# Optimization experiments

Hardware: AMD Instinct MI355X
Metric: run time of the kernel (lower is better)

Reference implementation:

```python
import jax, jax.numpy as jnp
import numpy as np

VOCAB, EMBED, HIDDEN = 32000, 256, 64
B, T = 4096, 64


def setup_inputs() -> dict:
    key = jax.random.key(0)
    ks = jax.random.split(key, 6)
    s = 1.0 / float(np.sqrt(HIDDEN))  # PyTorch LSTM init scale
    x = jax.random.randint(ks[0], (B, T), 0, VOCAB)
    embed_table = jax.random.normal(ks[1], (VOCAB, EMBED), jnp.float32)
    W_ih = jax.random.uniform(ks[2], (4 * HIDDEN, EMBED), jnp.float32, -s, s)
    W_hh = jax.random.uniform(ks[3], (4 * HIDDEN, HIDDEN), jnp.float32, -s, s)
    b_ih = jax.random.uniform(ks[4], (4 * HIDDEN,), jnp.float32, -s, s)
    b_hh = jax.random.uniform(ks[5], (4 * HIDDEN,), jnp.float32, -s, s)
    return {"x": x, "embed_table": embed_table, "W_ih": W_ih, "W_hh": W_hh, "b_ih": b_ih, "b_hh": b_hh}


def reference(x, embed_table, W_ih, W_hh, b_ih, b_hh):
    # Embedding lookup: [B,T,E]
    emb = embed_table[x]
    # Precompute input projection for all timesteps (PyTorch gate order i,f,g,o)
    xg = jnp.einsum('bte,ge->btg', emb, W_ih) + (b_ih + b_hh)  # [B,T,4H]
    xg = jnp.swapaxes(xg, 0, 1)  # [T,B,4H]
    h0 = jnp.zeros((x.shape[0], HIDDEN), xg.dtype)
    c0 = jnp.zeros((x.shape[0], HIDDEN), xg.dtype)

    def step(carry, xt):
        h, c = carry
        g = xt + h @ W_hh.T  # [B,4H]
        i, f, gg, o = jnp.split(g, 4, axis=-1)
        c = jax.nn.sigmoid(f) * c + jax.nn.sigmoid(i) * jnp.tanh(gg)
        h = jax.nn.sigmoid(o) * jnp.tanh(c)
        return (h, c), None

    (h, _), _ = jax.lax.scan(step, (h0, c0), xg)
    return h  # [B, HIDDEN] == hidden.squeeze(0)
```

## Files before the change

### kernel.cpp

```cpp
#include <hip/hip_runtime.h>
#include <math.h>

#define B_ 4096
#define T_ 64
#define E_ 256
#define H_ 64
#define V_ 32000
#define THREADS 1024

typedef __attribute__((ext_vector_type(8))) short bf16x8;
typedef __attribute__((ext_vector_type(4))) float f32x4;
typedef __attribute__((ext_vector_type(4))) unsigned int u32x4;

__device__ __forceinline__ short f2bf(float x) {
    unsigned u = __float_as_uint(x);
    return (short)((u + 0x7FFFu + ((u >> 16) & 1u)) >> 16);
}
__device__ __forceinline__ unsigned cvt_pk_bf16(float lo, float hi) {
    unsigned r;
    asm("v_cvt_pk_bf16_f32 %0, %1, %2" : "=v"(r) : "v"(lo), "v"(hi));
    return r;
}
__device__ __forceinline__ float exp2_raw(float x) {
    float r; asm("v_exp_f32 %0, %1" : "=v"(r) : "v"(x)); return r;
}
__device__ __forceinline__ float rcp_raw(float x) {
    float r; asm("v_rcp_f32 %0, %1" : "=v"(r) : "v"(x)); return r;
}
#define LOG2E 1.442695041f

__device__ __forceinline__ void gld16(const void* g, void* l) {
    __builtin_amdgcn_global_load_lds(
        (const __attribute__((address_space(1))) void*)g,
        (__attribute__((address_space(3))) void*)l, 16, 0, 0);
}

__global__ void prep_kernel(const float* __restrict__ W_ih,
                            const float* __restrict__ W_hh,
                            const float* __restrict__ b_ih,
                            const float* __restrict__ b_hh,
                            const float* __restrict__ emb_table,
                            short* __restrict__ wih_frag,
                            short* __restrict__ whh_g,
                            float* __restrict__ bias_f,
                            short* __restrict__ emb_bf,
                            int tabN) {
    int tid = blockIdx.x * blockDim.x + threadIdx.x;
    int stride = gridDim.x * blockDim.x;
    for (int i = tid; i < 65536; i += stride) {
        int jj = i & 7;
        int l  = (i >> 3) & 63;
        int kc = (i >> 9) & 7;
        int tl = (i >> 12) & 1;
        int vv = i >> 13;
        int uu = (l & 15) >> 1, pp = l & 1;
        int g = tl * 128 + pp * 64 + vv * 8 + uu;
        int k = kc * 32 + (l >> 4) * 8 + jj;
        wih_frag[i] = f2bf(W_ih[g * E_ + k]);
    }
    for (int i = tid; i < 256 * 64; i += stride) whh_g[i] = f2bf(W_hh[i]);
    for (int i = tid; i < 256; i += stride) bias_f[i] = b_ih[i] + b_hh[i];
    for (int i = tid; i < (tabN >> 2); i += stride) {
        float4 v = ((const float4*)emb_table)[i];
        uint2 w;
        w.x = cvt_pk_bf16(v.x, v.y);
        w.y = cvt_pk_bf16(v.z, v.w);
        ((uint2*)emb_bf)[i] = w;
    }
}

template <int TAB>
__global__ __attribute__((amdgpu_flat_work_group_size(THREADS, THREADS),
                          amdgpu_waves_per_eu(4, 4)))
void lstm_f(const int* __restrict__ x,
            const float* __restrict__ embf,
            const short* __restrict__ embb,
            const short* __restrict__ wih_frag,
            const short* __restrict__ whh_g,
            const float* __restrict__ bias_f,
            float* __restrict__ out) {
    __shared__ __align__(16) short s_ef[4][4096];
    __shared__ __align__(16) short s_hf[2][1024];
    __shared__ int s_idx[1024];

    const int tid  = threadIdx.x;
    const int lane = tid & 63;
    const int wave = tid >> 6;
    const int r0   = blockIdx.x * 16;

    s_idx[(tid & 63) * 16 + (tid >> 6)] = x[(r0 + (tid >> 6)) * T_ + (tid & 63)];
    ((int*)s_hf)[tid] = 0;

    const int p  = lane & 1;
    const int c4 = lane >> 4;
    const int u  = (lane & 15) >> 1;
    const float scl2 = p ? 1.0f : 2.0f;
    const float offB = p ? 0.0f : -1.0f;
    const float enB  = -LOG2E * scl2;
    const int m0 = c4 * 4 + p * 2;

    bf16x8 wA[8], wB[8], qA0, qA1, qB0, qB1;
    float bA = 0.f, bB = 0.f;
    int hw_s = 0;
    if (wave < 8) {
        const short* wp = wih_frag + wave * 8192 + lane * 8;
        #pragma unroll
        for (int kc = 0; kc < 8; ++kc) {
            wA[kc] = *(const bf16x8*)(wp + kc * 512);
            wB[kc] = *(const bf16x8*)(wp + 4096 + kc * 512);
        }
        const int gA = p * 64 + wave * 8 + u;
        const short* qp = whh_g + gA * 64 + c4 * 8;
        qA0 = *(const bf16x8*)(qp);
        qA1 = *(const bf16x8*)(qp + 32);
        qB0 = *(const bf16x8*)(qp + 8192);
        qB1 = *(const bf16x8*)(qp + 8192 + 32);
        bA = bias_f[gA];
        bB = bias_f[gA + 128];
        hw_s = (wave >> 2) * 512 + (wave & 3) * 128
             + ((u & 1) ? (m0 + 1) * 8 + (u - 1) : m0 * 8 + u);
    }

    const int m16   = lane & 15;
    const int sbase = (wave - 8) * 512 + lane * 8;
    const int skoff = (wave - 8) * 32 + (lane >> 4) * 8;

    __syncthreads();

    if (wave >= 8) {
        #pragma unroll
        for (int tt = 0; tt < 2; ++tt) {
            int tok = s_idx[tt * 16 + m16];
            if (TAB) {
                gld16(embb + (size_t)tok * E_ + skoff,
                      &s_ef[tt][(wave - 8) * 512]);
            } else {
                const float* pr = embf + (size_t)tok * E_ + skoff;
                float4 f0 = *(const float4*)pr;
                float4 f1 = *(const float4*)(pr + 4);
                u32x4 w;
                w[0] = cvt_pk_bf16(f0.x, f0.y);
                w[1] = cvt_pk_bf16(f0.z, f0.w);
                w[2] = cvt_pk_bf16(f1.x, f1.y);
                w[3] = cvt_pk_bf16(f1.z, f1.w);
                *(u32x4*)(&s_ef[tt][0] + sbase) = w;
            }
        }
    }
    __syncthreads();

    f32x4 pA, pB;
    if (wave < 8) {
        pA = (f32x4){bA, bA, bA, bA};
        pB = (f32x4){bB, bB, bB, bB};
        const short* eb = &s_ef[0][0] + lane * 8;
        #pragma unroll
        for (int kc = 0; kc < 8; ++kc) {
            bf16x8 av = *(const bf16x8*)(eb + kc * 512);
            pA = __builtin_amdgcn_mfma_f32_16x16x32_bf16(av, wA[kc], pA, 0, 0, 0);
            pB = __builtin_amdgcn_mfma_f32_16x16x32_bf16(av, wB[kc], pB, 0, 0, 0);
        }
    }

    float c0 = 0.f, c1 = 0.f, h0v = 0.f, h1v = 0.f;

    #pragma unroll 4
    for (int t = 0; t < T_; ++t) {
        if (wave < 8) {
            const short* hb = &s_hf[t & 1][0] + lane * 8;
            bf16x8 hv0 = *(const bf16x8*)(hb);
            bf16x8 hv1 = *(const bf16x8*)(hb + 512);
            pA = __builtin_amdgcn_mfma_f32_16x16x32_bf16(hv0, qA0, pA, 0, 0, 0);
            pA = __builtin_amdgcn_mfma_f32_16x16x32_bf16(hv1, qA1, pA, 0, 0, 0);
            pB = __builtin_amdgcn_mfma_f32_16x16x32_bf16(hv0, qB0, pB, 0, 0, 0);
            pB = __builtin_amdgcn_mfma_f32_16x16x32_bf16(hv1, qB1, pB, 0, 0, 0);

            float sA[4], Bv[4];
            #pragma unroll
            for (int q = 0; q < 4; ++q) {
                sA[q] = rcp_raw(1.0f + exp2_raw(-LOG2E * pA[q]));
                Bv[q] = rcp_raw(1.0f + exp2_raw(enB * pB[q])) * scl2 + offB;
            }
            float s1 = p ? sA[0] : sA[2] * Bv[2];
            float r1 = __shfl_xor(s1, 1);
            float s2 = p ? sA[1] : sA[3] * Bv[3];
            float r2 = __shfl_xor(s2, 1);
            float r3 = __shfl_xor(Bv[0], 1);
            float r4 = __shfl_xor(Bv[1], 1);
            float fc0 = p ? sA[2] : r1;
            float ic0 = p ? r1 : sA[0] * Bv[0];
            float oc0 = p ? Bv[2] : r3;
            float fc1 = p ? sA[3] : r2;
            float ic1 = p ? r2 : sA[1] * Bv[1];
            float oc1 = p ? Bv[3] : r4;
            c0 = fc0 * c0 + ic0;
            c1 = fc1 * c1 + ic1;
            h0v = oc0 * (1.0f - 2.0f * rcp_raw(1.0f + exp2_raw(2.0f * LOG2E * c0)));
            h1v = oc1 * (1.0f - 2.0f * rcp_raw(1.0f + exp2_raw(2.0f * LOG2E * c1)));

            float snd = (u & 1) ? h0v : h1v;
            float rcv = __shfl_xor(snd, 2);
            unsigned hw = (u & 1) ? cvt_pk_bf16(rcv, h1v) : cvt_pk_bf16(h0v, rcv);
            *(unsigned*)(&s_hf[(t + 1) & 1][0] + hw_s) = hw;

            if (t < T_ - 1) {
                pA = (f32x4){bA, bA, bA, bA};
                pB = (f32x4){bB, bB, bB, bB};
                const short* eb = &s_ef[(t + 1) & 3][0] + lane * 8;
                #pragma unroll
                for (int kc = 0; kc < 8; ++kc) {
                    bf16x8 av = *(const bf16x8*)(eb + kc * 512);
                    pA = __builtin_amdgcn_mfma_f32_16x16x32_bf16(av, wA[kc], pA, 0, 0, 0);
                    pB = __builtin_amdgcn_mfma_f32_16x16x32_bf16(av, wB[kc], pB, 0, 0, 0);
                }
            }
        } else {
            if (t + 2 < T_) {
                int tok = s_idx[(t + 2) * 16 + m16];
                if (TAB) {
                    gld16(embb + (size_t)tok * E_ + skoff,
                          &s_ef[(t + 2) & 3][(wave - 8) * 512]);
                } else {
                    const float* pr = embf + (size_t)tok * E_ + skoff;
                    float4 f0 = *(const float4*)pr;
                    float4 f1 = *(const float4*)(pr + 4);
                    u32x4 w;
                    w[0] = cvt_pk_bf16(f0.x, f0.y);
                    w[1] = cvt_pk_bf16(f0.z, f0.w);
                    w[2] = cvt_pk_bf16(f1.x, f1.y);
                    w[3] = cvt_pk_bf16(f1.z, f1.w);
                    *(u32x4*)(&s_ef[(t + 2) & 3][0] + sbase) = w;
                }
            }
        }
        __syncthreads();
    }

    if (wave < 8) {
        const int j = wave * 8 + u;
        out[(r0 + m0) * H_ + j]     = h0v;
        out[(r0 + m0 + 1) * H_ + j] = h1v;
    }
}

extern "C" void kernel_launch(void* const* d_in, const int* in_sizes, int n_in,
                              void* d_out, int out_size, void* d_ws, size_t ws_size,
                              hipStream_t stream) {
    const int*   x         = (const int*)d_in[0];
    const float* emb_table = (const float*)d_in[1];
    const float* W_ih      = (const float*)d_in[2];
    const float* W_hh      = (const float*)d_in[3];
    const float* b_ih      = (const float*)d_in[4];
    const float* b_hh      = (const float*)d_in[5];
    float*       out       = (float*)d_out;

    short* wih_frag = (short*)d_ws;
    short* whh_g    = wih_frag + 65536;
    float* bias_f   = (float*)(whh_g + 16384);
    short* emb_bf   = (short*)(bias_f + 256);

    const size_t need = (size_t)(65536 + 16384) * 2 + 256 * 4
                      + (size_t)V_ * E_ * 2;
    const int tab = (ws_size >= need) ? 1 : 0;

    prep_kernel<<<tab ? 1024 : 64, 256, 0, stream>>>(
        W_ih, W_hh, b_ih, b_hh, emb_table,
        wih_frag, whh_g, bias_f,
        tab ? emb_bf : wih_frag, tab ? V_ * E_ : 0);

    if (tab) {
        lstm_f<1><<<B_ / 16, THREADS, 0, stream>>>(
            x, emb_table, emb_bf, wih_frag, whh_g, bias_f, out);
    } else {
        lstm_f<0><<<B_ / 16, THREADS, 0, stream>>>(
            x, emb_table, wih_frag, wih_frag, whh_g, bias_f, out);
    }
}
```

Baseline: 75.05 us.

## Deepen embedding prefetch to three steps and split MFMA accumulators into two chains

The loader waves now prefetch embedding rows three timesteps ahead instead of two. On the async-load path, the full syncthreads is replaced by a partial vmcnt(1) wait plus a raw barrier, so one global load can stay in flight across the barrier. Each gate accumulator is split into two independent MFMA chains that are summed before the activations, which shortens the dependent MFMA chain on the recurrent critical path. This adds some VALU adds and registers, and it depends on the relaxed wait count being correct for the four-slot ring buffer.

```diff
diff --git a/kernel.cpp b/kernel.cpp
--- a/kernel.cpp
+++ b/kernel.cpp
@@ -129,7 +129,7 @@
 
     if (wave >= 8) {
         #pragma unroll
-        for (int tt = 0; tt < 2; ++tt) {
+        for (int tt = 0; tt < 3; ++tt) {
             int tok = s_idx[tt * 16 + m16];
             if (TAB) {
                 gld16(embb + (size_t)tok * E_ + skoff,
@@ -147,18 +147,29 @@
             }
         }
     }
-    __syncthreads();
-
-    f32x4 pA, pB;
+    if (TAB) {
+        asm volatile("s_waitcnt vmcnt(1) lgkmcnt(0)" ::: "memory");
+        __builtin_amdgcn_s_barrier();
+        __builtin_amdgcn_sched_barrier(0);
+    } else {
+        __syncthreads();
+    }
+
+    f32x4 a0, a1, b0, b1;
     if (wave < 8) {
-        pA = (f32x4){bA, bA, bA, bA};
-        pB = (f32x4){bB, bB, bB, bB};
+        a0 = (f32x4){bA, bA, bA, bA};
+        b0 = (f32x4){bB, bB, bB, bB};
+        a1 = (f32x4){0.f, 0.f, 0.f, 0.f};
+        b1 = (f32x4){0.f, 0.f, 0.f, 0.f};
         const short* eb = &s_ef[0][0] + lane * 8;
         #pragma unroll
-        for (int kc = 0; kc < 8; ++kc) {
+        for (int kc = 0; kc < 4; ++kc) {
             bf16x8 av = *(const bf16x8*)(eb + kc * 512);
-            pA = __builtin_amdgcn_mfma_f32_16x16x32_bf16(av, wA[kc], pA, 0, 0, 0);
-            pB = __builtin_amdgcn_mfma_f32_16x16x32_bf16(av, wB[kc], pB, 0, 0, 0);
+            bf16x8 aw = *(const bf16x8*)(eb + (kc + 4) * 512);
+            a0 = __builtin_amdgcn_mfma_f32_16x16x32_bf16(av, wA[kc], a0, 0, 0, 0);
+            b0 = __builtin_amdgcn_mfma_f32_16x16x32_bf16(av, wB[kc], b0, 0, 0, 0);
+            a1 = __builtin_amdgcn_mfma_f32_16x16x32_bf16(aw, wA[kc + 4], a1, 0, 0, 0);
+            b1 = __builtin_amdgcn_mfma_f32_16x16x32_bf16(aw, wB[kc + 4], b1, 0, 0, 0);
         }
     }
 
@@ -170,16 +181,18 @@
             const short* hb = &s_hf[t & 1][0] + lane * 8;
             bf16x8 hv0 = *(const bf16x8*)(hb);
             bf16x8 hv1 = *(const bf16x8*)(hb + 512);
-            pA = __builtin_amdgcn_mfma_f32_16x16x32_bf16(hv0, qA0, pA, 0, 0, 0);
-            pA = __builtin_amdgcn_mfma_f32_16x16x32_bf16(hv1, qA1, pA, 0, 0, 0);
-            pB = __builtin_amdgcn_mfma_f32_16x16x32_bf16(hv0, qB0, pB, 0, 0, 0);
-            pB = __builtin_amdgcn_mfma_f32_16x16x32_bf16(hv1, qB1, pB, 0, 0, 0);
+            a0 = __builtin_amdgcn_mfma_f32_16x16x32_bf16(hv0, qA0, a0, 0, 0, 0);
+            a1 = __builtin_amdgcn_mfma_f32_16x16x32_bf16(hv1, qA1, a1, 0, 0, 0);
+            b0 = __builtin_amdgcn_mfma_f32_16x16x32_bf16(hv0, qB0, b0, 0, 0, 0);
+            b1 = __builtin_amdgcn_mfma_f32_16x16x32_bf16(hv1, qB1, b1, 0, 0, 0);
 
             float sA[4], Bv[4];
             #pragma unroll
             for (int q = 0; q < 4; ++q) {
-                sA[q] = rcp_raw(1.0f + exp2_raw(-LOG2E * pA[q]));
-                Bv[q] = rcp_raw(1.0f + exp2_raw(enB * pB[q])) * scl2 + offB;
+                float gaq = a0[q] + a1[q];
+                float gbq = b0[q] + b1[q];
+                sA[q] = rcp_raw(1.0f + exp2_raw(-LOG2E * gaq));
+                Bv[q] = rcp_raw(1.0f + exp2_raw(enB * gbq)) * scl2 + offB;
             }
             float s1 = p ? sA[0] : sA[2] * Bv[2];
             float r1 = __shfl_xor(s1, 1);
@@ -204,22 +217,27 @@
             *(unsigned*)(&s_hf[(t + 1) & 1][0] + hw_s) = hw;
 
             if (t < T_ - 1) {
-                pA = (f32x4){bA, bA, bA, bA};
-                pB = (f32x4){bB, bB, bB, bB};
+                a0 = (f32x4){bA, bA, bA, bA};
+                b0 = (f32x4){bB, bB, bB, bB};
+                a1 = (f32x4){0.f, 0.f, 0.f, 0.f};
+                b1 = (f32x4){0.f, 0.f, 0.f, 0.f};
                 const short* eb = &s_ef[(t + 1) & 3][0] + lane * 8;
                 #pragma unroll
-                for (int kc = 0; kc < 8; ++kc) {
+                for (int kc = 0; kc < 4; ++kc) {
                     bf16x8 av = *(const bf16x8*)(eb + kc * 512);
-                    pA = __builtin_amdgcn_mfma_f32_16x16x32_bf16(av, wA[kc], pA, 0, 0, 0);
-                    pB = __builtin_amdgcn_mfma_f32_16x16x32_bf16(av, wB[kc], pB, 0, 0, 0);
+                    bf16x8 aw = *(const bf16x8*)(eb + (kc + 4) * 512);
+                    a0 = __builtin_amdgcn_mfma_f32_16x16x32_bf16(av, wA[kc], a0, 0, 0, 0);
+                    b0 = __builtin_amdgcn_mfma_f32_16x16x32_bf16(av, wB[kc], b0, 0, 0, 0);
+                    a1 = __builtin_amdgcn_mfma_f32_16x16x32_bf16(aw, wA[kc + 4], a1, 0, 0, 0);
+                    b1 = __builtin_amdgcn_mfma_f32_16x16x32_bf16(aw, wB[kc + 4], b1, 0, 0, 0);
                 }
             }
         } else {
-            if (t + 2 < T_) {
-                int tok = s_idx[(t + 2) * 16 + m16];
+            if (t + 3 < T_) {
+                int tok = s_idx[(t + 3) * 16 + m16];
                 if (TAB) {
                     gld16(embb + (size_t)tok * E_ + skoff,
-                          &s_ef[(t + 2) & 3][(wave - 8) * 512]);
+                          &s_ef[(t + 3) & 3][(wave - 8) * 512]);
                 } else {
                     const float* pr = embf + (size_t)tok * E_ + skoff;
                     float4 f0 = *(const float4*)pr;
@@ -229,11 +247,17 @@
                     w[1] = cvt_pk_bf16(f0.z, f0.w);
                     w[2] = cvt_pk_bf16(f1.x, f1.y);
                     w[3] = cvt_pk_bf16(f1.z, f1.w);
-                    *(u32x4*)(&s_ef[(t + 2) & 3][0] + sbase) = w;
+                    *(u32x4*)(&s_ef[(t + 3) & 3][0] + sbase) = w;
                 }
             }
         }
-        __syncthreads();
+        if (TAB) {
+            asm volatile("s_waitcnt vmcnt(1) lgkmcnt(0)" ::: "memory");
+            __builtin_amdgcn_s_barrier();
+            __builtin_amdgcn_sched_barrier(0);
+        } else {
+            __syncthreads();
+        }
     }
 
     if (wave < 8) {
```

After: 93.95 us. +25.2%, slower.
